# Optimization experiments

Measured on AMD Instinct MI355X. Metric: run time of the kernel, lower is better.

Reference implementation:

```python
import jax, jax.numpy as jnp
import numpy as np

N = 100000
E = 1600000
VOCAB = 16
D = 128   # node_embedding_dim == hidden_channels
NUM_LAYERS = 3


def setup_inputs() -> dict:
    key = jax.random.key(0)
    ks = jax.random.split(key, 12)
    x = jax.random.randint(ks[0], (N, 1), 0, VOCAB, dtype=jnp.int64) if jax.config.jax_enable_x64 else jax.random.randint(ks[0], (N, 1), 0, VOCAB, dtype=jnp.int32)
    edge_index = jax.random.randint(ks[1], (2, E), 0, N, dtype=jnp.int32)
    s = 1.0 / np.sqrt(D)
    inp = {
        "x": x,
        "edge_index": edge_index,
        "emb": jax.random.normal(ks[2], (VOCAB, D), jnp.float32),
        "W0": jax.random.normal(ks[3], (D, D), jnp.float32) * s,
        "b0": jnp.zeros((D,), jnp.float32),
        "W1": jax.random.normal(ks[4], (D, D), jnp.float32) * s,
        "b1": jnp.zeros((D,), jnp.float32),
        "W2": jax.random.normal(ks[5], (D, D), jnp.float32) * s,
        "b2": jnp.zeros((D,), jnp.float32),
        "Wm1": jax.random.normal(ks[6], (2 * D, D), jnp.float32) * (1.0 / np.sqrt(2 * D)),
        "bm1": jnp.zeros((D,), jnp.float32),
        "Wm2": jax.random.normal(ks[7], (D, 3), jnp.float32) * s,
        "bm2": jnp.zeros((3,), jnp.float32),
    }
    return inp


def _gcn_conv(h, src_sl, dst_sl, norm, W, b):
    # PyG GCNConv: x' = scatter_dst(norm * (x W)[src]) + b, with self-loops included
    hW = h @ W                                   # [N, D]
    msg = hW[src_sl] * norm[:, None]             # [(E+N), D] gather
    agg = jax.ops.segment_sum(msg, dst_sl, num_segments=N)  # scatter-add
    return agg + b


def reference(x, edge_index, emb, W0, b0, W1, b1, W2, b2, Wm1, bm1, Wm2, bm2):
    src, dst = edge_index[0], edge_index[1]
    # add self-loops
    loop = jnp.arange(N, dtype=src.dtype)
    src_sl = jnp.concatenate([src, loop])
    dst_sl = jnp.concatenate([dst, loop])
    # symmetric degree normalization: deg counted on dst (col)
    deg = jax.ops.segment_sum(jnp.ones_like(dst_sl, jnp.float32), dst_sl, num_segments=N)
    dis = jnp.where(deg > 0, jax.lax.rsqrt(jnp.maximum(deg, 1.0)), 0.0)
    norm = dis[src_sl] * dis[dst_sl]             # [(E+N)]

    # node encoder: embedding lookup (dropout omitted: eval mode)
    h = emb[x[:, 0]]                             # [N, D]
    for W, b in ((W0, b0), (W1, b1), (W2, b2)):
        h = jax.nn.relu(_gcn_conv(h, src_sl, dst_sl, norm, W, b))

    # edge classifier: gather endpoints, concat, MLP
    ef = jnp.concatenate([h[src], h[dst]], axis=-1)   # [E, 2D]
    hid = jax.nn.relu(ef @ Wm1 + bm1)
    return hid @ Wm2 + bm2                             # [E, 3]
```

## Files before the change

kernel.cpp:

```cpp
#include <hip/hip_runtime.h>
#include <hip/hip_bf16.h>

#define N_NODES 100000
#define N_EDGES 1600000


__global__ void hist_k(const int* __restrict__ ei, int* __restrict__ cnt, int E) {
    int e = blockIdx.x * 256 + threadIdx.x;
    if (e < E) atomicAdd(&cnt[ei[E + e]], 1);
}

__global__ void scan_cnt_k(const int* __restrict__ cnt, const int* __restrict__ x,
                           int* __restrict__ offs, int* __restrict__ bsum,
                           float* __restrict__ dis, int* __restrict__ sxp, int n) {
    __shared__ int buf[2][256];
    int t = threadIdx.x;
    int i = blockIdx.x * 256 + t;
    int v = (i < n) ? cnt[i] : 0;
    if (i < n) {
        float d = rsqrtf(1.0f + (float)v);
        dis[i] = d;
        sxp[i] = (__float_as_int(d) & ~15) | x[i];
    }
    int p = 0;
    buf[0][t] = v;
    __syncthreads();
    for (int off = 1; off < 256; off <<= 1) {
        int nv = buf[p][t];
        if (t >= off) nv += buf[p][t - off];
        buf[p ^ 1][t] = nv;
        p ^= 1;
        __syncthreads();
    }
    if (i < n) offs[i] = buf[p][t] - v;
    if (t == 255) bsum[blockIdx.x] = buf[p][t];
}

__global__ void scan_bsum_k(int* __restrict__ bsum, int nb) {
    __shared__ int buf[2][512];
    int t = threadIdx.x;
    int v = (t < nb) ? bsum[t] : 0;
    int p = 0;
    buf[0][t] = v;
    __syncthreads();
    for (int off = 1; off < 512; off <<= 1) {
        int nv = buf[p][t];
        if (t >= off) nv += buf[p][t - off];
        buf[p ^ 1][t] = nv;
        p ^= 1;
        __syncthreads();
    }
    if (t < nb) bsum[t] = buf[p][t] - v;
}

__global__ void scan_add_k(int* __restrict__ offs, int* __restrict__ cursor,
                           const int* __restrict__ bsum, int n, int total) {
    int i = blockIdx.x * 256 + threadIdx.x;
    if (i < n) {
        int o = offs[i] + bsum[blockIdx.x];
        offs[i] = o;
        cursor[i] = o;
    }
    if (i == 0) offs[n] = total;
}

__global__ void fill_csr_k(const int* __restrict__ ei, int* __restrict__ cursor,
                           int* __restrict__ srcs, int* __restrict__ eid, int E) {
    int e = blockIdx.x * 256 + threadIdx.x;
    if (e < E) {
        int s = ei[e];
        int d = ei[E + e];
        int pos = atomicAdd(&cursor[d], 1);
        srcs[pos] = s;
        eid[pos] = e;
    }
}


__global__ void t0_k(const float* __restrict__ emb, const float* __restrict__ W0,
                     float* __restrict__ T0) {
    int v = blockIdx.x;
    int c = threadIdx.x;
    float acc = 0.f;
    for (int k = 0; k < 128; ++k) acc += emb[v * 128 + k] * W0[k * 128 + c];
    T0[v * 128 + c] = acc;
}

__global__ __launch_bounds__(256) void vgather_k(const int* __restrict__ sxp,
                                                 const int* __restrict__ offs,
                                                 const int* __restrict__ srcs,
                                                 const float* __restrict__ dis,
                                                 const float* __restrict__ T0,
                                                 const float* __restrict__ b0,
                                                 float* __restrict__ h, int n) {
    __shared__ float t0s[16 * 128];
    __shared__ float cv[4][16];
    int t = threadIdx.x;
    #pragma unroll
    for (int i = 0; i < 8; ++i) t0s[t + i * 256] = T0[t + i * 256];
    if (t < 64) cv[t >> 4][t & 15] = 0.f;
    __syncthreads();

    int w = t >> 6, lane = t & 63;
    int node = blockIdx.x * 4 + w;
    float di = dis[node];
    int j0 = offs[node], j1 = offs[node + 1];
    for (int j = j0 + lane; j < j1; j += 64) {
        int b = sxp[srcs[j]];
        atomicAdd(&cv[w][b & 15], __int_as_float(b));
    }
    if (lane == 0) atomicAdd(&cv[w][sxp[node] & 15], di);
    __syncthreads();

    float2 acc = make_float2(0.f, 0.f);
    #pragma unroll
    for (int v = 0; v < 16; ++v) {
        float c = cv[w][v];
        float2 tv = *(const float2*)&t0s[v * 128 + lane * 2];
        acc.x += c * tv.x;
        acc.y += c * tv.y;
    }
    float2 bb = *(const float2*)&b0[lane * 2];
    float2 r = make_float2(fmaxf(di * acc.x + bb.x, 0.f),
                           fmaxf(di * acc.y + bb.y, 0.f));
    ((float2*)h)[(size_t)node * 64 + lane] = r;
}


__global__ __launch_bounds__(256) void matmul128_k(const float* __restrict__ in,
                                                   const float* __restrict__ W,
                                                   float* __restrict__ out,
                                                   const float* __restrict__ scale,
                                                   int n) {
    __shared__ float hlds[64][132];
    int t = threadIdx.x;
    int row0 = blockIdx.x * 64;
    #pragma unroll
    for (int it = 0; it < 8; ++it) {
        int i4 = t + it * 256;
        int r = i4 >> 5, c4 = (i4 & 31) << 2;
        float4 v = make_float4(0.f, 0.f, 0.f, 0.f);
        int g = row0 + r;
        if (g < n) v = *(const float4*)&in[(size_t)g * 128 + c4];
        *(float4*)&hlds[r][c4] = v;
    }
    __syncthreads();
    int cg = t & 31, rg = t >> 5;
    int c0 = cg << 2;
    float acc[8][4];
    #pragma unroll
    for (int r = 0; r < 8; ++r)
        for (int j = 0; j < 4; ++j) acc[r][j] = 0.f;
    #pragma unroll 4
    for (int k = 0; k < 128; ++k) {
        float4 w = *(const float4*)&W[(size_t)k * 128 + c0];
        #pragma unroll
        for (int r = 0; r < 8; ++r) {
            float hk = hlds[rg * 8 + r][k];
            acc[r][0] += hk * w.x;
            acc[r][1] += hk * w.y;
            acc[r][2] += hk * w.z;
            acc[r][3] += hk * w.w;
        }
    }
    #pragma unroll
    for (int r = 0; r < 8; ++r) {
        int g = row0 + rg * 8 + r;
        if (g < n) {
            float sc = scale[g];
            float4 o = make_float4(acc[r][0] * sc, acc[r][1] * sc,
                                   acc[r][2] * sc, acc[r][3] * sc);
            *(float4*)&out[(size_t)g * 128 + c0] = o;
        }
    }
}

__global__ __launch_bounds__(256) void matmulAB_k(const float* __restrict__ in,
                                                  const float* __restrict__ WA,
                                                  const float* __restrict__ WB,
                                                  float* __restrict__ outA,
                                                  float* __restrict__ outB, int n) {
    __shared__ float hlds[64][132];
    int t = threadIdx.x;
    int row0 = blockIdx.x * 64;
    #pragma unroll
    for (int it = 0; it < 8; ++it) {
        int i4 = t + it * 256;
        int r = i4 >> 5, c4 = (i4 & 31) << 2;
        float4 v = make_float4(0.f, 0.f, 0.f, 0.f);
        int g = row0 + r;
        if (g < n) v = *(const float4*)&in[(size_t)g * 128 + c4];
        *(float4*)&hlds[r][c4] = v;
    }
    __syncthreads();
    int cg = t & 31, rg = t >> 5;
    int c0 = cg << 2;
    float accA[8][4], accB[8][4];
    #pragma unroll
    for (int r = 0; r < 8; ++r)
        for (int j = 0; j < 4; ++j) { accA[r][j] = 0.f; accB[r][j] = 0.f; }
    #pragma unroll 2
    for (int k = 0; k < 128; ++k) {
        float4 wa = *(const float4*)&WA[(size_t)k * 128 + c0];
        float4 wb = *(const float4*)&WB[(size_t)k * 128 + c0];
        #pragma unroll
        for (int r = 0; r < 8; ++r) {
            float hk = hlds[rg * 8 + r][k];
            accA[r][0] += hk * wa.x;
            accA[r][1] += hk * wa.y;
            accA[r][2] += hk * wa.z;
            accA[r][3] += hk * wa.w;
            accB[r][0] += hk * wb.x;
            accB[r][1] += hk * wb.y;
            accB[r][2] += hk * wb.z;
            accB[r][3] += hk * wb.w;
        }
    }
    #pragma unroll
    for (int r = 0; r < 8; ++r) {
        int g = row0 + rg * 8 + r;
        if (g < n) {
            *(float4*)&outA[(size_t)g * 128 + c0] = *(float4*)&accA[r][0];
            *(float4*)&outB[(size_t)g * 128 + c0] = *(float4*)&accB[r][0];
        }
    }
}

__global__ __launch_bounds__(256) void gcn_gather_k(const float* __restrict__ hW,
                                                    const int* __restrict__ offs,
                                                    const int* __restrict__ srcs,
                                                    const float* __restrict__ dis,
                                                    const float* __restrict__ bias,
                                                    float* __restrict__ hout, int n) {
    int t = threadIdx.x;
    int node = blockIdx.x * 4 + (t >> 6);
    int lane = t & 63;
    int g = lane >> 3, sl = lane & 7;
    const float4* hw4 = (const float4*)hW;
    size_t selfrb = (size_t)node * 32 + sl;
    float4 a[4];
    if (g == 0) {
        #pragma unroll
        for (int k = 0; k < 4; ++k) a[k] = hw4[selfrb + 8 * k];
    } else {
        #pragma unroll
        for (int k = 0; k < 4; ++k) a[k] = make_float4(0.f, 0.f, 0.f, 0.f);
    }
    int j0 = offs[node], j1 = offs[node + 1];
    for (int j = j0 + g; j < j1; j += 8) {
        size_t rb = (size_t)srcs[j] * 32 + sl;
        #pragma unroll
        for (int k = 0; k < 4; ++k) {
            float4 u = hw4[rb + 8 * k];
            a[k].x += u.x; a[k].y += u.y; a[k].z += u.z; a[k].w += u.w;
        }
    }
    #pragma unroll
    for (int m = 8; m <= 32; m <<= 1) {
        #pragma unroll
        for (int k = 0; k < 4; ++k) {
            a[k].x += __shfl_xor(a[k].x, m);
            a[k].y += __shfl_xor(a[k].y, m);
            a[k].z += __shfl_xor(a[k].z, m);
            a[k].w += __shfl_xor(a[k].w, m);
        }
    }
    if (g == 0) {
        float di = dis[node];
        #pragma unroll
        for (int k = 0; k < 4; ++k) {
            float4 bb = ((const float4*)bias)[sl + 8 * k];
            float4 r = make_float4(fmaxf(di * a[k].x + bb.x, 0.f),
                                   fmaxf(di * a[k].y + bb.y, 0.f),
                                   fmaxf(di * a[k].z + bb.z, 0.f),
                                   fmaxf(di * a[k].w + bb.w, 0.f));
            ((float4*)hout)[selfrb + 8 * k] = r;
        }
    }
}

__global__ __launch_bounds__(256) void edge_mlp_k(const int* __restrict__ offs,
                                                  const int* __restrict__ srcs,
                                                  const int* __restrict__ eid,
                                                  const float* __restrict__ A,
                                                  const float* __restrict__ B,
                                                  const float* __restrict__ Wm2,
                                                  const float* __restrict__ bm1,
                                                  const float* __restrict__ bm2,
                                                  float* __restrict__ out, int n) {
    int t = threadIdx.x;
    int node = blockIdx.x * 4 + (t >> 6);
    int lane = t & 63;
    int g = lane >> 4, sl = lane & 15;
    int j0 = offs[node], j1 = offs[node + 1];
    if (j0 == j1) return;

    const float4* B4 = (const float4*)(B + (size_t)node * 128 + sl * 8);
    const float4* bm14 = (const float4*)(bm1 + sl * 8);
    float4 pre0 = B4[0], pre1 = B4[1];
    float4 m0 = bm14[0], m1 = bm14[1];
    pre0.x += m0.x; pre0.y += m0.y; pre0.z += m0.z; pre0.w += m0.w;
    pre1.x += m1.x; pre1.y += m1.y; pre1.z += m1.z; pre1.w += m1.w;

    float wv[8][3];
    #pragma unroll
    for (int i = 0; i < 8; ++i) {
        int f = sl * 8 + i;
        wv[i][0] = Wm2[f * 3 + 0];
        wv[i][1] = Wm2[f * 3 + 1];
        wv[i][2] = Wm2[f * 3 + 2];
    }
    float c0 = bm2[0], c1 = bm2[1], c2 = bm2[2];

    for (int jb = j0; jb < j1; jb += 4) {
        int jj = jb + g;
        bool act = jj < j1;
        int jsafe = act ? jj : j0;
        int s = srcs[jsafe];
        int e = eid[jsafe];
        const float4* A4 = (const float4*)(A + (size_t)s * 128 + sl * 8);
        float4 a0 = A4[0], a1 = A4[1];
        float h[8];
        h[0] = fmaxf(a0.x + pre0.x, 0.f);
        h[1] = fmaxf(a0.y + pre0.y, 0.f);
        h[2] = fmaxf(a0.z + pre0.z, 0.f);
        h[3] = fmaxf(a0.w + pre0.w, 0.f);
        h[4] = fmaxf(a1.x + pre1.x, 0.f);
        h[5] = fmaxf(a1.y + pre1.y, 0.f);
        h[6] = fmaxf(a1.z + pre1.z, 0.f);
        h[7] = fmaxf(a1.w + pre1.w, 0.f);
        float p0 = 0.f, p1 = 0.f, p2 = 0.f;
        #pragma unroll
        for (int i = 0; i < 8; ++i) {
            p0 += h[i] * wv[i][0];
            p1 += h[i] * wv[i][1];
            p2 += h[i] * wv[i][2];
        }
        #pragma unroll
        for (int m = 1; m <= 8; m <<= 1) {
            p0 += __shfl_xor(p0, m);
            p1 += __shfl_xor(p1, m);
            p2 += __shfl_xor(p2, m);
        }
        if (act && sl == 0) {
            out[(size_t)e * 3 + 0] = p0 + c0;
            out[(size_t)e * 3 + 1] = p1 + c1;
            out[(size_t)e * 3 + 2] = p2 + c2;
        }
    }
}

extern "C" void kernel_launch(void* const* d_in, const int* in_sizes, int n_in,
                              void* d_out, int out_size, void* d_ws, size_t ws_size,
                              hipStream_t stream) {
    const int N = N_NODES, E = N_EDGES;
    const int* x    = (const int*)d_in[0];
    const int* ei   = (const int*)d_in[1];
    const float* emb = (const float*)d_in[2];
    const float* W0 = (const float*)d_in[3];
    const float* b0 = (const float*)d_in[4];
    const float* W1 = (const float*)d_in[5];
    const float* b1 = (const float*)d_in[6];
    const float* W2 = (const float*)d_in[7];
    const float* b2 = (const float*)d_in[8];
    const float* Wm1 = (const float*)d_in[9];
    const float* bm1 = (const float*)d_in[10];
    const float* Wm2 = (const float*)d_in[11];
    const float* bm2 = (const float*)d_in[12];
    float* out = (float*)d_out;

    char* p = (char*)d_ws;
    auto alloc = [&](size_t bytes) {
        char* r = p;
        p += (bytes + 511) & ~(size_t)511;
        return r;
    };
    int*    cnt    = (int*)alloc((size_t)N * 4);
    float*  dis    = (float*)alloc((size_t)N * 4);
    int*    sxp    = (int*)alloc((size_t)N * 4);
    int*    offs   = (int*)alloc((size_t)(N + 1) * 4);
    int*    cursor = (int*)alloc((size_t)N * 4);
    int*    bsum   = (int*)alloc(512 * 4);
    int*    srcs   = (int*)alloc((size_t)E * 4);
    int*    eid    = (int*)alloc((size_t)E * 4);
    float*  T0     = (float*)alloc(16 * 128 * 4);
    float*  buf0   = (float*)alloc((size_t)N * 128 * 4);
    float*  buf1   = (float*)alloc((size_t)N * 128 * 4);
    float*  buf2   = (float*)alloc((size_t)N * 128 * 4);

    int nbN = (N + 255) / 256;
    int nbE = (E + 255) / 256;
    int nodeBlocks = N / 4;
    int mmBlocks = (N + 63) / 64;

    hipMemsetAsync(cnt, 0, (size_t)N * 4, stream);
    hist_k<<<nbE, 256, 0, stream>>>(ei, cnt, E);
    scan_cnt_k<<<nbN, 256, 0, stream>>>(cnt, x, offs, bsum, dis, sxp, N);
    scan_bsum_k<<<1, 512, 0, stream>>>(bsum, nbN);
    scan_add_k<<<nbN, 256, 0, stream>>>(offs, cursor, bsum, N, E);
    fill_csr_k<<<nbE, 256, 0, stream>>>(ei, cursor, srcs, eid, E);

    t0_k<<<16, 128, 0, stream>>>(emb, W0, T0);
    vgather_k<<<nodeBlocks, 256, 0, stream>>>(sxp, offs, srcs, dis, T0, b0, buf0, N);

    const float* Ws[2] = {W1, W2};
    const float* bs[2] = {b1, b2};
    for (int l = 0; l < 2; ++l) {
        matmul128_k<<<mmBlocks, 256, 0, stream>>>(buf0, Ws[l], buf1, dis, N);
        gcn_gather_k<<<nodeBlocks, 256, 0, stream>>>(buf1, offs, srcs, dis, bs[l], buf0, N);
    }

    matmulAB_k<<<mmBlocks, 256, 0, stream>>>(buf0, Wm1, Wm1 + 128 * 128, buf1, buf2, N);

    edge_mlp_k<<<nodeBlocks, 256, 0, stream>>>(offs, srcs, eid, buf1, buf2, Wm2, bm1, bm2, out, N);
}
```

Measured before the change: 812.6 us.

## Fuse GCN neighbor gather into following matmul via LDS tile

Merges the per-node CSR gather/aggregate (with bias and ReLU) directly into the next layer's dense matmul, writing aggregated rows into a shared-memory tile instead of global memory. This removes two kernel launches and a full N×128 write plus read of the intermediate hidden state for layers 2 and the edge-MLP projection. In exchange, each 256-thread block now gathers 64 nodes with only 4 wavefronts, with 1563 blocks instead of 25000, so it has less parallelism and latency hiding for the irregular gather.

```diff
diff --git a/kernel.cpp b/kernel.cpp
--- a/kernel.cpp
+++ b/kernel.cpp
@@ -175,23 +175,113 @@
     }
 }
 
-__global__ __launch_bounds__(256) void matmulAB_k(const float* __restrict__ in,
-                                                  const float* __restrict__ WA,
-                                                  const float* __restrict__ WB,
-                                                  float* __restrict__ outA,
-                                                  float* __restrict__ outB, int n) {
+
+__device__ __forceinline__ void gather_tile_to_lds(
+    const float4* __restrict__ hw4, const int* __restrict__ offs,
+    const int* __restrict__ srcs, const float* __restrict__ dis,
+    const float* __restrict__ bias, float hlds[64][132],
+    int row0, int n, int t) {
+    int w = t >> 6, lane = t & 63;
+    int g = lane >> 3, sl = lane & 7;
+    float4 bb[4];
+    #pragma unroll
+    for (int k = 0; k < 4; ++k) bb[k] = ((const float4*)bias)[sl + 8 * k];
+    for (int i = 0; i < 16; ++i) {
+        int nl = (w << 4) + i;
+        int node = row0 + nl;
+        if (node >= n) break;
+        size_t selfrb = (size_t)node * 32 + sl;
+        float4 a[4];
+        if (g == 0) {
+            #pragma unroll
+            for (int k = 0; k < 4; ++k) a[k] = hw4[selfrb + 8 * k];
+        } else {
+            #pragma unroll
+            for (int k = 0; k < 4; ++k) a[k] = make_float4(0.f, 0.f, 0.f, 0.f);
+        }
+        int j0 = offs[node], j1 = offs[node + 1];
+        for (int j = j0 + g; j < j1; j += 8) {
+            size_t rb = (size_t)srcs[j] * 32 + sl;
+            #pragma unroll
+            for (int k = 0; k < 4; ++k) {
+                float4 u = hw4[rb + 8 * k];
+                a[k].x += u.x; a[k].y += u.y; a[k].z += u.z; a[k].w += u.w;
+            }
+        }
+        #pragma unroll
+        for (int m = 8; m <= 32; m <<= 1) {
+            #pragma unroll
+            for (int k = 0; k < 4; ++k) {
+                a[k].x += __shfl_xor(a[k].x, m);
+                a[k].y += __shfl_xor(a[k].y, m);
+                a[k].z += __shfl_xor(a[k].z, m);
+                a[k].w += __shfl_xor(a[k].w, m);
+            }
+        }
+        if (g == 0) {
+            float di = dis[node];
+            #pragma unroll
+            for (int k = 0; k < 4; ++k) {
+                float4 r = make_float4(fmaxf(di * a[k].x + bb[k].x, 0.f),
+                                       fmaxf(di * a[k].y + bb[k].y, 0.f),
+                                       fmaxf(di * a[k].z + bb[k].z, 0.f),
+                                       fmaxf(di * a[k].w + bb[k].w, 0.f));
+                *(float4*)&hlds[nl][(sl + 8 * k) * 4] = r;
+            }
+        }
+    }
+}
+
+__global__ __launch_bounds__(256) void fused_gm_k(
+    const float* __restrict__ hWin, const int* __restrict__ offs,
+    const int* __restrict__ srcs, const float* __restrict__ dis,
+    const float* __restrict__ bias, const float* __restrict__ W,
+    float* __restrict__ out, int n) {
     __shared__ float hlds[64][132];
     int t = threadIdx.x;
     int row0 = blockIdx.x * 64;
-    #pragma unroll
-    for (int it = 0; it < 8; ++it) {
-        int i4 = t + it * 256;
-        int r = i4 >> 5, c4 = (i4 & 31) << 2;
-        float4 v = make_float4(0.f, 0.f, 0.f, 0.f);
-        int g = row0 + r;
-        if (g < n) v = *(const float4*)&in[(size_t)g * 128 + c4];
-        *(float4*)&hlds[r][c4] = v;
-    }
+    gather_tile_to_lds((const float4*)hWin, offs, srcs, dis, bias, hlds, row0, n, t);
+    __syncthreads();
+    int cg = t & 31, rg = t >> 5;
+    int c0 = cg << 2;
+    float acc[8][4];
+    #pragma unroll
+    for (int r = 0; r < 8; ++r)
+        for (int j = 0; j < 4; ++j) acc[r][j] = 0.f;
+    #pragma unroll 4
+    for (int k = 0; k < 128; ++k) {
+        float4 w = *(const float4*)&W[(size_t)k * 128 + c0];
+        #pragma unroll
+        for (int r = 0; r < 8; ++r) {
+            float hk = hlds[rg * 8 + r][k];
+            acc[r][0] += hk * w.x;
+            acc[r][1] += hk * w.y;
+            acc[r][2] += hk * w.z;
+            acc[r][3] += hk * w.w;
+        }
+    }
+    #pragma unroll
+    for (int r = 0; r < 8; ++r) {
+        int gr = row0 + rg * 8 + r;
+        if (gr < n) {
+            float sc = dis[gr];
+            float4 o = make_float4(acc[r][0] * sc, acc[r][1] * sc,
+                                   acc[r][2] * sc, acc[r][3] * sc);
+            *(float4*)&out[(size_t)gr * 128 + c0] = o;
+        }
+    }
+}
+
+__global__ __launch_bounds__(256) void fused_gm2_k(
+    const float* __restrict__ hWin, const int* __restrict__ offs,
+    const int* __restrict__ srcs, const float* __restrict__ dis,
+    const float* __restrict__ bias, const float* __restrict__ WA,
+    const float* __restrict__ WB, float* __restrict__ outA,
+    float* __restrict__ outB, int n) {
+    __shared__ float hlds[64][132];
+    int t = threadIdx.x;
+    int row0 = blockIdx.x * 64;
+    gather_tile_to_lds((const float4*)hWin, offs, srcs, dis, bias, hlds, row0, n, t);
     __syncthreads();
     int cg = t & 31, rg = t >> 5;
     int c0 = cg << 2;
@@ -218,63 +308,10 @@
     }
     #pragma unroll
     for (int r = 0; r < 8; ++r) {
-        int g = row0 + rg * 8 + r;
-        if (g < n) {
-            *(float4*)&outA[(size_t)g * 128 + c0] = *(float4*)&accA[r][0];
-            *(float4*)&outB[(size_t)g * 128 + c0] = *(float4*)&accB[r][0];
-        }
-    }
-}
-
-__global__ __launch_bounds__(256) void gcn_gather_k(const float* __restrict__ hW,
-                                                    const int* __restrict__ offs,
-                                                    const int* __restrict__ srcs,
-                                                    const float* __restrict__ dis,
-                                                    const float* __restrict__ bias,
-                                                    float* __restrict__ hout, int n) {
-    int t = threadIdx.x;
-    int node = blockIdx.x * 4 + (t >> 6);
-    int lane = t & 63;
-    int g = lane >> 3, sl = lane & 7;
-    const float4* hw4 = (const float4*)hW;
-    size_t selfrb = (size_t)node * 32 + sl;
-    float4 a[4];
-    if (g == 0) {
-        #pragma unroll
-        for (int k = 0; k < 4; ++k) a[k] = hw4[selfrb + 8 * k];
-    } else {
-        #pragma unroll
-        for (int k = 0; k < 4; ++k) a[k] = make_float4(0.f, 0.f, 0.f, 0.f);
-    }
-    int j0 = offs[node], j1 = offs[node + 1];
-    for (int j = j0 + g; j < j1; j += 8) {
-        size_t rb = (size_t)srcs[j] * 32 + sl;
-        #pragma unroll
-        for (int k = 0; k < 4; ++k) {
-            float4 u = hw4[rb + 8 * k];
-            a[k].x += u.x; a[k].y += u.y; a[k].z += u.z; a[k].w += u.w;
-        }
-    }
-    #pragma unroll
-    for (int m = 8; m <= 32; m <<= 1) {
-        #pragma unroll
-        for (int k = 0; k < 4; ++k) {
-            a[k].x += __shfl_xor(a[k].x, m);
-            a[k].y += __shfl_xor(a[k].y, m);
-            a[k].z += __shfl_xor(a[k].z, m);
-            a[k].w += __shfl_xor(a[k].w, m);
-        }
-    }
-    if (g == 0) {
-        float di = dis[node];
-        #pragma unroll
-        for (int k = 0; k < 4; ++k) {
-            float4 bb = ((const float4*)bias)[sl + 8 * k];
-            float4 r = make_float4(fmaxf(di * a[k].x + bb.x, 0.f),
-                                   fmaxf(di * a[k].y + bb.y, 0.f),
-                                   fmaxf(di * a[k].z + bb.z, 0.f),
-                                   fmaxf(di * a[k].w + bb.w, 0.f));
-            ((float4*)hout)[selfrb + 8 * k] = r;
+        int gr = row0 + rg * 8 + r;
+        if (gr < n) {
+            *(float4*)&outA[(size_t)gr * 128 + c0] = *(float4*)&accA[r][0];
+            *(float4*)&outB[(size_t)gr * 128 + c0] = *(float4*)&accB[r][0];
         }
     }
 }
@@ -403,14 +440,10 @@
     t0_k<<<16, 128, 0, stream>>>(emb, W0, T0);
     vgather_k<<<nodeBlocks, 256, 0, stream>>>(sxp, offs, srcs, dis, T0, b0, buf0, N);
 
-    const float* Ws[2] = {W1, W2};
-    const float* bs[2] = {b1, b2};
-    for (int l = 0; l < 2; ++l) {
-        matmul128_k<<<mmBlocks, 256, 0, stream>>>(buf0, Ws[l], buf1, dis, N);
-        gcn_gather_k<<<nodeBlocks, 256, 0, stream>>>(buf1, offs, srcs, dis, bs[l], buf0, N);
-    }
-
-    matmulAB_k<<<mmBlocks, 256, 0, stream>>>(buf0, Wm1, Wm1 + 128 * 128, buf1, buf2, N);
+    matmul128_k<<<mmBlocks, 256, 0, stream>>>(buf0, W1, buf1, dis, N);
+    fused_gm_k<<<mmBlocks, 256, 0, stream>>>(buf1, offs, srcs, dis, b1, W2, buf0, N);
+    fused_gm2_k<<<mmBlocks, 256, 0, stream>>>(buf0, offs, srcs, dis, b2,
+                                              Wm1, Wm1 + 128 * 128, buf1, buf2, N);
 
     edge_mlp_k<<<nodeBlocks, 256, 0, stream>>>(offs, srcs, eid, buf1, buf2, Wm2, bm1, bm2, out, N);
 }
```

New measurement: 809.7 us. No clear change (-0.4%).
